# Kernel tuning notes

Measured on AMD Instinct MI355X. Metric: run time of the kernel, lower is better.

Reference implementation:

```python
import jax, jax.numpy as jnp
import numpy as np
from jax.scipy.special import xlogy

W_BI = 0.5
W_TRI = 0.5
EPS = 1e-10


def setup_inputs() -> dict:
    key = jax.random.key(0)
    B, L, V = 8, 2048, 512
    logits = jax.random.normal(key, (B, L, V), dtype=jnp.float32)
    return {"logits": logits}


def _safe_normalized_entropy(joint, max_log):
    # 1 - H(joint)/H_max (concentration penalty), fp32-safe
    joint = joint / (joint.sum() + EPS)
    entropy = -xlogy(joint, jnp.clip(joint, EPS, None)).sum()
    return jnp.clip(1.0 - entropy / (max_log + EPS), 0.0, 1.0)


def reference(logits):
    x = jnp.nan_to_num(logits.astype(jnp.float32), nan=0.0, posinf=80.0, neginf=-80.0)
    p = jax.nn.softmax(x, axis=-1)  # (B, L, V)
    B, L, V = p.shape
    max_log_bi = float(np.log(float(V * V)))
    max_log_tri = float(np.log(float(V) ** 3))

    total = jnp.zeros((), dtype=jnp.float32)

    # Bigram joint distribution over (V, V)
    bigram_joint = jnp.einsum('nla,nlb->ab', p[:, :-1, :], p[:, 1:, :])
    total = total + W_BI * _safe_normalized_entropy(bigram_joint, max_log_bi)

    # Trigram: (V,V) bigram part outer-producted with third-position marginal -> (V,V,V)
    bi_part = jnp.einsum('nla,nlb->ab', p[:, :-2, :], p[:, 1:-1, :])
    tri_joint = jnp.einsum('ab,nlc->abc', bi_part, p[:, 2:, :])
    total = total + W_TRI * _safe_normalized_entropy(tri_joint, max_log_tri)

    return jnp.clip(jnp.nan_to_num(total, nan=0.0, posinf=1.0), 0.0, 1.0)
```

## Files before the change

kernel.cpp:

```cpp
#include <hip/hip_runtime.h>
#include <math.h>

#define L_SEQ 2048
#define V 512
#define NROWS 16384
#define LDT 16392
#define NSPLIT 32
#define EPS 1e-10

typedef __bf16 bf16x8 __attribute__((ext_vector_type(8)));
typedef float f32x4 __attribute__((ext_vector_type(4)));

#define PT_OFF  ((size_t)0)
#define GP_OFF  ((size_t)512 * LDT * 2)
#define RB_OFF  (GP_OFF + (size_t)NSPLIT * V * V * 4)
#define M_OFF   (RB_OFF + (size_t)23 * V * 4)
#define PC_OFF  (M_OFF + (size_t)V * 4)

#define GLDS16(g, l) __builtin_amdgcn_global_load_lds( \
    (const __attribute__((address_space(1))) unsigned int*)(g), \
    (__attribute__((address_space(3))) unsigned int*)(l), 16, 0, 0)

__device__ __forceinline__ unsigned short f2bf(float f) {
    unsigned u = __float_as_uint(f);
    unsigned r = (u + 0x7fffu + ((u >> 16) & 1u)) >> 16;
    return (unsigned short)r;
}

__device__ __forceinline__ void softmax_row_bf16(const float* __restrict__ x,
                                                 int lane, unsigned short* out) {
    float4 va = *(const float4*)(x + lane * 4);
    float4 vb = *(const float4*)(x + 256 + lane * 4);
    float v[8] = {va.x, va.y, va.z, va.w, vb.x, vb.y, vb.z, vb.w};
#pragma unroll
    for (int i = 0; i < 8; i++) {
        float xi = v[i];
        if (isnan(xi)) xi = 0.0f;
        else if (isinf(xi)) xi = xi > 0.0f ? 80.0f : -80.0f;
        v[i] = xi;
    }
    float mx = v[0];
#pragma unroll
    for (int i = 1; i < 8; i++) mx = fmaxf(mx, v[i]);
#pragma unroll
    for (int o = 32; o; o >>= 1) mx = fmaxf(mx, __shfl_xor(mx, o, 64));
    float e[8];
    float s = 0.0f;
#pragma unroll
    for (int i = 0; i < 8; i++) { e[i] = expf(v[i] - mx); s += e[i]; }
#pragma unroll
    for (int o = 32; o; o >>= 1) s += __shfl_xor(s, o, 64);
    float inv = 1.0f / s;
#pragma unroll
    for (int i = 0; i < 8; i++) out[i] = f2bf(e[i] * inv);
}

__global__ __launch_bounds__(256) void softmaxT_k(const float* __restrict__ in,
                                                  unsigned short* __restrict__ pT) {
    __shared__ __align__(16) unsigned short sm[32 * 512];
    int t = threadIdx.x;
    int w = t >> 6, lane = t & 63;
    int k0 = blockIdx.x * 32;
#pragma unroll
    for (int i = 0; i < 8; i++) {
        int rr = w * 8 + i;
        unsigned short o[8];
        softmax_row_bf16(in + (size_t)(k0 + rr) * V, lane, o);
        *(ushort4*)&sm[rr * 512 + lane * 4] = make_ushort4(o[0], o[1], o[2], o[3]);
        *(ushort4*)&sm[rr * 512 + 256 + lane * 4] = make_ushort4(o[4], o[5], o[6], o[7]);
    }
    __syncthreads();
    int v0 = 2 * t;
    unsigned u[32];
#pragma unroll
    for (int k = 0; k < 32; k++) u[k] = *(const unsigned*)&sm[k * 512 + v0];
    unsigned oA[16], oB[16];
#pragma unroll
    for (int i = 0; i < 16; i++) {
        unsigned e0 = u[2 * i], e1 = u[2 * i + 1];
        oA[i] = (e0 & 0xffffu) | (e1 << 16);
        oB[i] = (e0 >> 16) | (e1 & 0xffff0000u);
    }
    uint4* dA = (uint4*)(pT + (size_t)v0 * LDT + k0);
    uint4* dB = (uint4*)(pT + (size_t)(v0 + 1) * LDT + k0);
#pragma unroll
    for (int i = 0; i < 4; i++) {
        dA[i] = make_uint4(oA[4 * i], oA[4 * i + 1], oA[4 * i + 2], oA[4 * i + 3]);
        dB[i] = make_uint4(oB[4 * i], oB[4 * i + 1], oB[4 * i + 2], oB[4 * i + 3]);
    }
    if (blockIdx.x == 511) {
        *(uint4*)(pT + (size_t)v0 * LDT + 16384) = make_uint4(0, 0, 0, 0);
        *(uint4*)(pT + (size_t)(v0 + 1) * LDT + 16384) = make_uint4(0, 0, 0, 0);
    }
}

__global__ __launch_bounds__(64) void rows_k(const float* __restrict__ in,
                                             float* __restrict__ rb) {
    int j = blockIdx.x, lane = threadIdx.x;
    int r = j < 8 ? j * L_SEQ + L_SEQ - 2
          : j < 16 ? (j - 8) * L_SEQ + L_SEQ - 1
          : (j - 15) * L_SEQ;
    unsigned short o[8];
    softmax_row_bf16(in + (size_t)r * V, lane, o);
#pragma unroll
    for (int i = 0; i < 4; i++)
        rb[j * V + lane * 4 + i] = __uint_as_float((unsigned)o[i] << 16);
#pragma unroll
    for (int i = 0; i < 4; i++)
        rb[j * V + 256 + lane * 4 + i] = __uint_as_float((unsigned)o[4 + i] << 16);
}

__global__ __launch_bounds__(256) void colsum_k(const unsigned short* __restrict__ pT,
                                                float* __restrict__ m) {
    int c = blockIdx.x, t = threadIdx.x;
    const unsigned short* row = pT + (size_t)c * LDT;
    float s = 0.0f;
#pragma unroll
    for (int j = 0; j < 8; j++) {
        int g = t + 256 * j;
        uint4 x = *(const uint4*)(row + g * 8);
        float partial = 0.0f;
        unsigned ww[4] = {x.x, x.y, x.z, x.w};
#pragma unroll
        for (int qq = 0; qq < 4; qq++) {
            partial += __uint_as_float(ww[qq] << 16);
            partial += __uint_as_float(ww[qq] & 0xffff0000u);
        }
        if ((g & 255) == 0)
            partial -= __uint_as_float(ww[0] << 16) + __uint_as_float(ww[0] & 0xffff0000u);
        s += partial;
    }
#pragma unroll
    for (int o = 32; o; o >>= 1) s += __shfl_xor(s, o, 64);
    __shared__ float red[4];
    if ((t & 63) == 0) red[t >> 6] = s;
    __syncthreads();
    if (t == 0) m[c] = red[0] + red[1] + red[2] + red[3];
}

__global__ __launch_bounds__(256) void gemm_k(const unsigned short* __restrict__ pT,
                                              float* __restrict__ gp) {
    __shared__ __align__(16) uint4 ldsA[512];
    __shared__ __align__(16) uint4 ldsB[512];
    int tile = blockIdx.x & 15, split = blockIdx.x >> 4;
    int ta = (tile >> 2) * 128, tb = (tile & 3) * 128;
    int t = threadIdx.x, w = t >> 6, lane = t & 63;
    int l15 = lane & 15, q = lane >> 4;
    int wa = (w & 1) * 64, wb = (w >> 1) * 64;
    int k0base = split * 512;

    f32x4 acc[4][4];
#pragma unroll
    for (int g = 0; g < 4; g++)
#pragma unroll
        for (int h = 0; h < 4; h++) acc[g][h] = (f32x4){0.f, 0.f, 0.f, 0.f};

    int srow = 16 * w + (lane >> 2);
    int qoff = (lane & 3) * 8;
    const size_t rA1 = (size_t)(ta + srow) * LDT;
    const size_t rA2 = (size_t)(ta + 64 + srow) * LDT;
    const size_t rB1 = (size_t)(tb + srow) * LDT;
    const size_t rB2 = (size_t)(tb + 64 + srow) * LDT;

    for (int it = 0; it < 16; it++) {
        int kel = k0base + it * 32 + qoff;
        const unsigned short* gb1 = pT + rB1 + kel;
        const unsigned short* gb2 = pT + rB2 + kel;
        uint4 x1 = *(const uint4*)gb1;
        unsigned y1 = *(const unsigned*)(gb1 + 8);
        uint4 x2 = *(const uint4*)gb2;
        unsigned y2 = *(const unsigned*)(gb2 + 8);
        __syncthreads();
        GLDS16(pT + rA1 + kel, &ldsA[64 * w]);
        GLDS16(pT + rA2 + kel, &ldsA[256 + 64 * w]);
        uint4 s1, s2;
        s1.x = (x1.x >> 16) | (x1.y << 16);
        s1.y = (x1.y >> 16) | (x1.z << 16);
        s1.z = (x1.z >> 16) | (x1.w << 16);
        s1.w = (x1.w >> 16) | (y1 << 16);
        s2.x = (x2.x >> 16) | (x2.y << 16);
        s2.y = (x2.y >> 16) | (x2.z << 16);
        s2.z = (x2.z >> 16) | (x2.w << 16);
        s2.w = (x2.w >> 16) | (y2 << 16);
        ldsB[64 * w + lane] = s1;
        ldsB[256 + 64 * w + lane] = s2;
        __syncthreads();
        bf16x8 af[4], bv[4];
#pragma unroll
        for (int g = 0; g < 4; g++)
            af[g] = __builtin_bit_cast(bf16x8, ldsA[4 * (wa + g * 16 + l15) + q]);
#pragma unroll
        for (int h = 0; h < 4; h++)
            bv[h] = __builtin_bit_cast(bf16x8, ldsB[4 * (wb + h * 16 + l15) + q]);
#pragma unroll
        for (int g = 0; g < 4; g++)
#pragma unroll
            for (int h = 0; h < 4; h++)
                acc[g][h] = __builtin_amdgcn_mfma_f32_16x16x32_bf16(af[g], bv[h], acc[g][h], 0, 0, 0);
    }

    float* og = gp + (size_t)split * V * V;
#pragma unroll
    for (int g = 0; g < 4; g++) {
        int a = ta + wa + g * 16 + q * 4;
#pragma unroll
        for (int h = 0; h < 4; h++) {
            int b = tb + wb + h * 16 + l15;
#pragma unroll
            for (int r = 0; r < 4; r++)
                og[(size_t)(a + r) * V + b] = acc[g][h][r];
        }
    }
}

__global__ __launch_bounds__(256) void reduceg_k(const float* __restrict__ gp,
                                                 const float* __restrict__ rb,
                                                 double* __restrict__ pc) {
    int t = threadIdx.x;
    int idx = blockIdx.x * 256 + t;
    int a = idx >> 9, b = idx & (V - 1);
    double ga = 0, gb2 = 0, gc = 0, gd = 0;
#pragma unroll
    for (int s = 0; s < NSPLIT; s += 4) {
        ga += (double)gp[(size_t)(s + 0) * V * V + idx];
        gb2 += (double)gp[(size_t)(s + 1) * V * V + idx];
        gc += (double)gp[(size_t)(s + 2) * V * V + idx];
        gd += (double)gp[(size_t)(s + 3) * V * V + idx];
    }
    double g = (ga + gb2) + (gc + gd);
    float cross = 0.f, cc = 0.f;
#pragma unroll
    for (int n = 0; n < 7; n++)
        cross = fmaf(rb[(8 + n) * V + a], rb[(16 + n) * V + b], cross);
#pragma unroll
    for (int n = 0; n < 8; n++)
        cc = fmaf(rb[n * V + a], rb[(8 + n) * V + b], cc);
    double g1 = g - (double)cross;
    double g2 = g1 - (double)cc;
    double s1 = g1, t1 = g1 * (double)logf((float)g1);
    double s2 = g2, t2 = g2 * (double)logf((float)g2);
#pragma unroll
    for (int o = 32; o; o >>= 1) {
        s1 += __shfl_xor(s1, o, 64);
        t1 += __shfl_xor(t1, o, 64);
        s2 += __shfl_xor(s2, o, 64);
        t2 += __shfl_xor(t2, o, 64);
    }
    __shared__ double red[4][4];
    if ((t & 63) == 0) {
        int w = t >> 6;
        red[w][0] = s1; red[w][1] = t1; red[w][2] = s2; red[w][3] = t2;
    }
    __syncthreads();
    if (t == 0) {
        double* o = pc + (size_t)blockIdx.x * 4;
        o[0] = red[0][0] + red[1][0] + red[2][0] + red[3][0];
        o[1] = red[0][1] + red[1][1] + red[2][1] + red[3][1];
        o[2] = red[0][2] + red[1][2] + red[2][2] + red[3][2];
        o[3] = red[0][3] + red[1][3] + red[2][3] + red[3][3];
    }
}

__global__ __launch_bounds__(512) void final_k(const float* __restrict__ m,
                                               const double* __restrict__ pc,
                                               float* __restrict__ out) {
    int t = threadIdx.x;
    double s1 = 0, t1 = 0, s2 = 0, t2 = 0;
#pragma unroll
    for (int j = 0; j < 2; j++) {
        const double* q = pc + (size_t)(t + 512 * j) * 4;
        s1 += q[0]; t1 += q[1]; s2 += q[2]; t2 += q[3];
    }
    double mv = (double)m[t];
    double sm = mv;
    double tm = mv * log(mv);
#pragma unroll
    for (int o = 32; o; o >>= 1) {
        sm += __shfl_xor(sm, o, 64);
        tm += __shfl_xor(tm, o, 64);
        s1 += __shfl_xor(s1, o, 64);
        t1 += __shfl_xor(t1, o, 64);
        s2 += __shfl_xor(s2, o, 64);
        t2 += __shfl_xor(t2, o, 64);
    }
    __shared__ double red[6][8];
    if ((t & 63) == 0) {
        int w = t >> 6;
        red[0][w] = sm; red[1][w] = tm;
        red[2][w] = s1; red[3][w] = t1;
        red[4][w] = s2; red[5][w] = t2;
    }
    __syncthreads();
    if (t == 0) {
        double acc[6];
        for (int i = 0; i < 6; i++) {
            acc[i] = 0;
            for (int w = 0; w < 8; w++) acc[i] += red[i][w];
        }
        double Sm = acc[0], Tm = acc[1];
        double S1 = acc[2], T1 = acc[3], S2 = acc[4], T2 = acc[5];
        double D1 = S1 + EPS;
        double Hbi = (log(D1) * S1 - T1) / D1;
        double mlb = log((double)V * (double)V);
        double cbi = 1.0 - Hbi / (mlb + EPS);
        cbi = fmin(fmax(cbi, 0.0), 1.0);
        double S3 = S2 * Sm;
        double D3 = S3 + EPS;
        double Htri = (log(D3) * S3 - (Sm * T2 + S2 * Tm)) / D3;
        double mlt = log((double)V * (double)V * (double)V);
        double ctri = 1.0 - Htri / (mlt + EPS);
        ctri = fmin(fmax(ctri, 0.0), 1.0);
        double tot = 0.5 * cbi + 0.5 * ctri;
        if (!(tot == tot)) tot = 0.0;
        tot = fmin(fmax(tot, 0.0), 1.0);
        out[0] = (float)tot;
    }
}

extern "C" void kernel_launch(void* const* d_in, const int* in_sizes, int n_in,
                              void* d_out, int out_size, void* d_ws, size_t ws_size,
                              hipStream_t stream) {
    (void)in_sizes; (void)n_in; (void)out_size; (void)ws_size;
    const float* logits = (const float*)d_in[0];
    float* out = (float*)d_out;
    char* ws = (char*)d_ws;
    unsigned short* pT = (unsigned short*)(ws + PT_OFF);
    float* gp = (float*)(ws + GP_OFF);
    float* rb = (float*)(ws + RB_OFF);
    float* m = (float*)(ws + M_OFF);
    double* pc = (double*)(ws + PC_OFF);

    softmaxT_k<<<512, 256, 0, stream>>>(logits, pT);
    rows_k<<<23, 64, 0, stream>>>(logits, rb);
    colsum_k<<<512, 256, 0, stream>>>(pT, m);
    gemm_k<<<512, 256, 0, stream>>>(pT, gp);
    reduceg_k<<<1024, 256, 0, stream>>>(gp, rb, pc);
    final_k<<<1, 512, 0, stream>>>(m, pc, out);
}
```

Before: 131.6 us.

## Fuse column-sum into softmax-transpose kernel with atomics, drop colsum kernel

The per-vocab column sums are now accumulated inside the softmax/transpose kernel and added with float atomics, so the separate colsum kernel that re-read the whole transposed bf16 matrix is removed. Each block now handles 64 rows instead of 32, which halves the grid and doubles shared memory, and the leading dimension is padded to 16448 with a wider zero tail. This saves a full pass over pT and one launch, at the cost of a memset, 512 atomics per block, and lower occupancy in the softmax kernel. The padding change may also shift bank and channel conflicts in the GEMM loads.

```diff
diff --git a/kernel.cpp b/kernel.cpp
--- a/kernel.cpp
+++ b/kernel.cpp
@@ -4,7 +4,7 @@
 #define L_SEQ 2048
 #define V 512
 #define NROWS 16384
-#define LDT 16392
+#define LDT 16448
 #define NSPLIT 32
 #define EPS 1e-10
 
@@ -56,14 +56,15 @@
 }
 
 __global__ __launch_bounds__(256) void softmaxT_k(const float* __restrict__ in,
-                                                  unsigned short* __restrict__ pT) {
-    __shared__ __align__(16) unsigned short sm[32 * 512];
+                                                  unsigned short* __restrict__ pT,
+                                                  float* __restrict__ m) {
+    __shared__ __align__(16) unsigned short sm[64 * 512];
     int t = threadIdx.x;
     int w = t >> 6, lane = t & 63;
-    int k0 = blockIdx.x * 32;
-#pragma unroll
-    for (int i = 0; i < 8; i++) {
-        int rr = w * 8 + i;
+    int k0 = blockIdx.x * 64;
+#pragma unroll
+    for (int i = 0; i < 16; i++) {
+        int rr = w * 16 + i;
         unsigned short o[8];
         softmax_row_bf16(in + (size_t)(k0 + rr) * V, lane, o);
         *(ushort4*)&sm[rr * 512 + lane * 4] = make_ushort4(o[0], o[1], o[2], o[3]);
@@ -71,26 +72,42 @@
     }
     __syncthreads();
     int v0 = 2 * t;
-    unsigned u[32];
-#pragma unroll
-    for (int k = 0; k < 32; k++) u[k] = *(const unsigned*)&sm[k * 512 + v0];
-    unsigned oA[16], oB[16];
-#pragma unroll
-    for (int i = 0; i < 16; i++) {
-        unsigned e0 = u[2 * i], e1 = u[2 * i + 1];
-        oA[i] = (e0 & 0xffffu) | (e1 << 16);
-        oB[i] = (e0 >> 16) | (e1 & 0xffff0000u);
-    }
-    uint4* dA = (uint4*)(pT + (size_t)v0 * LDT + k0);
-    uint4* dB = (uint4*)(pT + (size_t)(v0 + 1) * LDT + k0);
-#pragma unroll
-    for (int i = 0; i < 4; i++) {
-        dA[i] = make_uint4(oA[4 * i], oA[4 * i + 1], oA[4 * i + 2], oA[4 * i + 3]);
-        dB[i] = make_uint4(oB[4 * i], oB[4 * i + 1], oB[4 * i + 2], oB[4 * i + 3]);
-    }
-    if (blockIdx.x == 511) {
-        *(uint4*)(pT + (size_t)v0 * LDT + 16384) = make_uint4(0, 0, 0, 0);
-        *(uint4*)(pT + (size_t)(v0 + 1) * LDT + 16384) = make_uint4(0, 0, 0, 0);
+    float mA = 0.0f, mB = 0.0f;
+    bool excl = ((k0 & (L_SEQ - 1)) == 0);
+#pragma unroll
+    for (int h = 0; h < 2; h++) {
+        unsigned u[32];
+#pragma unroll
+        for (int k = 0; k < 32; k++) u[k] = *(const unsigned*)&sm[(32 * h + k) * 512 + v0];
+#pragma unroll
+        for (int k = 0; k < 32; k++) {
+            if (h == 0 && excl && k < 2) continue;
+            mA += __uint_as_float(u[k] << 16);
+            mB += __uint_as_float(u[k] & 0xffff0000u);
+        }
+        unsigned oA[16], oB[16];
+#pragma unroll
+        for (int i = 0; i < 16; i++) {
+            unsigned e0 = u[2 * i], e1 = u[2 * i + 1];
+            oA[i] = (e0 & 0xffffu) | (e1 << 16);
+            oB[i] = (e0 >> 16) | (e1 & 0xffff0000u);
+        }
+        uint4* dA = (uint4*)(pT + (size_t)v0 * LDT + k0 + 32 * h);
+        uint4* dB = (uint4*)(pT + (size_t)(v0 + 1) * LDT + k0 + 32 * h);
+#pragma unroll
+        for (int i = 0; i < 4; i++) {
+            dA[i] = make_uint4(oA[4 * i], oA[4 * i + 1], oA[4 * i + 2], oA[4 * i + 3]);
+            dB[i] = make_uint4(oB[4 * i], oB[4 * i + 1], oB[4 * i + 2], oB[4 * i + 3]);
+        }
+    }
+    atomicAdd(&m[v0], mA);
+    atomicAdd(&m[v0 + 1], mB);
+    if (blockIdx.x == 255) {
+#pragma unroll
+        for (int j = 0; j < 8; j++) {
+            *(uint4*)(pT + (size_t)v0 * LDT + 16384 + 8 * j) = make_uint4(0, 0, 0, 0);
+            *(uint4*)(pT + (size_t)(v0 + 1) * LDT + 16384 + 8 * j) = make_uint4(0, 0, 0, 0);
+        }
     }
 }
 
@@ -108,34 +125,6 @@
 #pragma unroll
     for (int i = 0; i < 4; i++)
         rb[j * V + 256 + lane * 4 + i] = __uint_as_float((unsigned)o[4 + i] << 16);
-}
-
-__global__ __launch_bounds__(256) void colsum_k(const unsigned short* __restrict__ pT,
-                                                float* __restrict__ m) {
-    int c = blockIdx.x, t = threadIdx.x;
-    const unsigned short* row = pT + (size_t)c * LDT;
-    float s = 0.0f;
-#pragma unroll
-    for (int j = 0; j < 8; j++) {
-        int g = t + 256 * j;
-        uint4 x = *(const uint4*)(row + g * 8);
-        float partial = 0.0f;
-        unsigned ww[4] = {x.x, x.y, x.z, x.w};
-#pragma unroll
-        for (int qq = 0; qq < 4; qq++) {
-            partial += __uint_as_float(ww[qq] << 16);
-            partial += __uint_as_float(ww[qq] & 0xffff0000u);
-        }
-        if ((g & 255) == 0)
-            partial -= __uint_as_float(ww[0] << 16) + __uint_as_float(ww[0] & 0xffff0000u);
-        s += partial;
-    }
-#pragma unroll
-    for (int o = 32; o; o >>= 1) s += __shfl_xor(s, o, 64);
-    __shared__ float red[4];
-    if ((t & 63) == 0) red[t >> 6] = s;
-    __syncthreads();
-    if (t == 0) m[c] = red[0] + red[1] + red[2] + red[3];
 }
 
 __global__ __launch_bounds__(256) void gemm_k(const unsigned short* __restrict__ pT,
@@ -330,9 +319,9 @@
     float* m = (float*)(ws + M_OFF);
     double* pc = (double*)(ws + PC_OFF);
 
-    softmaxT_k<<<512, 256, 0, stream>>>(logits, pT);
+    (void)hipMemsetAsync(m, 0, V * sizeof(float), stream);
+    softmaxT_k<<<256, 256, 0, stream>>>(logits, pT, m);
     rows_k<<<23, 64, 0, stream>>>(logits, rb);
-    colsum_k<<<512, 256, 0, stream>>>(pT, m);
     gemm_k<<<512, 256, 0, stream>>>(pT, gp);
     reduceg_k<<<1024, 256, 0, stream>>>(gp, rb, pc);
     final_k<<<1, 512, 0, stream>>>(m, pc, out);
```

Result: slower. 141.0 us (+7.2%).
